# Optimization experiments

Hardware: AMD Instinct MI355X
Metric: run time of the kernel (lower is better)

Reference implementation:

```python
import jax, jax.numpy as jnp
import numpy as np

B, LS, LT = 32, 64, 64
V_SRC, V_TGT = 32000, 32000
E, H = 512, 512


def setup_inputs() -> dict:
    key = jax.random.key(0)
    ks = jax.random.split(key, 16)
    s = 0.05
    inp = {
        "src": jax.random.randint(ks[0], (B, LS), 0, V_SRC),
        "tgt": jax.random.randint(ks[1], (B, LT), 0, V_TGT),
        # encoder params
        "enc_embed": jax.random.normal(ks[2], (V_SRC, E), jnp.float32) * s,
        "enc_wih": jax.random.normal(ks[3], (E, H), jnp.float32) * s,
        "enc_bih": jax.random.normal(ks[4], (H,), jnp.float32) * s,
        "enc_whh": jax.random.normal(ks[5], (H, H), jnp.float32) * s,
        "enc_bhh": jax.random.normal(ks[6], (H,), jnp.float32) * s,
        # decoder params
        "dec_embed": jax.random.normal(ks[7], (V_TGT, E), jnp.float32) * s,
        "dec_wih": jax.random.normal(ks[8], (E, H), jnp.float32) * s,
        "dec_bih": jax.random.normal(ks[9], (H,), jnp.float32) * s,
        "dec_whh": jax.random.normal(ks[10], (H, H), jnp.float32) * s,
        "dec_bhh": jax.random.normal(ks[11], (H,), jnp.float32) * s,
        "h2o_w": jax.random.normal(ks[12], (H, V_TGT), jnp.float32) * s,
        "h2o_b": jax.random.normal(ks[13], (V_TGT,), jnp.float32) * s,
    }
    return inp


def _rnn_scan(tokens, embed, wih, bih, whh, bhh, h0):
    # tokens: (N, L) int; returns (final hidden (N,H), all hiddens (L,N,H))
    xs = embed[tokens].transpose(1, 0, 2)  # (L, N, E)

    def step(h, x):
        h = jnp.tanh(x @ wih + bih + h @ whh + bhh)
        return h, h

    h_last, hs = jax.lax.scan(step, h0, xs)
    return h_last, hs


def reference(src, tgt, enc_embed, enc_wih, enc_bih, enc_whh, enc_bhh,
              dec_embed, dec_wih, dec_bih, dec_whh, dec_bhh, h2o_w, h2o_b):
    n = src.shape[0]
    h0 = jnp.zeros((n, enc_whh.shape[0]), dtype=enc_whh.dtype)
    # encoder: tanh RNN over src, keep only final hidden (teacher-forced training path)
    hidden, _ = _rnn_scan(src, enc_embed, enc_wih, enc_bih, enc_whh, enc_bhh, h0)
    # decoder: tanh RNN over tgt with teacher forcing
    _, dec_hs = _rnn_scan(tgt, dec_embed, dec_wih, dec_bih, dec_whh, dec_bhh, hidden)  # (Lt, N, H)
    # per-step h2o + LogSoftmax, batched over all steps at once (same math)
    logits = dec_hs @ h2o_w + h2o_b  # (Lt, N, V)
    outputs = jax.nn.log_softmax(logits, axis=-1).transpose(1, 0, 2)  # (N, Lt, V)
    return outputs
```

## Files before the change

kernel.cpp:

```cpp
#include <hip/hip_runtime.h>

#define Bd 32
#define Ld 64
#define Hd 512
#define Vd 32000

typedef __bf16 bf16_t;
typedef __bf16 bf16x8 __attribute__((ext_vector_type(8)));
typedef float  f32x4  __attribute__((ext_vector_type(4)));

__global__ void k_pre(
    const int* __restrict__ src, const int* __restrict__ tgt,
    const float* __restrict__ enc_embed, const float* __restrict__ enc_wih,
    const float* __restrict__ enc_bih, const float* __restrict__ enc_bhh,
    const float* __restrict__ dec_embed, const float* __restrict__ dec_wih,
    const float* __restrict__ dec_bih, const float* __restrict__ dec_bhh,
    float* __restrict__ Aenc, float* __restrict__ Adec)
{
    const int tid = threadIdx.x;
    const int bid = blockIdx.x;
    __shared__ float sm[16 * Hd];
    __shared__ int tokl[16];

    const bool isDec = bid >= 128;
    const int rb = (isDec ? bid - 128 : bid) << 4;
    const int*   toks = isDec ? tgt : src;
    const float* emb  = isDec ? dec_embed : enc_embed;
    const float* wih  = isDec ? dec_wih : enc_wih;
    const float* bi   = isDec ? dec_bih : enc_bih;
    const float* bh   = isDec ? dec_bhh : enc_bhh;
    float*       A    = isDec ? Adec : Aenc;
    if (tid < 16) {
        int r = rb + tid;
        tokl[tid] = toks[(r & 31) * Ld + (r >> 5)];
    }
    __syncthreads();
    #pragma unroll
    for (int u = 0; u < 8; ++u) {
        int f = tid + (u << 8);
        int row = f >> 7, c4 = f & 127;
        ((float4*)sm)[f] = ((const float4*)(emb + (size_t)tokl[row] * Hd))[c4];
    }
    __syncthreads();
    const int j0 = tid, j1 = tid + 256;
    float acc0[16], acc1[16];
    #pragma unroll
    for (int r = 0; r < 16; ++r) { acc0[r] = 0.f; acc1[r] = 0.f; }
    #pragma unroll 4
    for (int k = 0; k < Hd; ++k) {
        float w0 = wih[(size_t)k * Hd + j0];
        float w1 = wih[(size_t)k * Hd + j1];
        #pragma unroll
        for (int r = 0; r < 16; ++r) {
            float x = sm[r * Hd + k];
            acc0[r] += x * w0;
            acc1[r] += x * w1;
        }
    }
    float bb0 = bi[j0] + bh[j0], bb1 = bi[j1] + bh[j1];
    #pragma unroll
    for (int r = 0; r < 16; ++r) {
        A[(size_t)(rb + r) * Hd + j0] = acc0[r] + bb0;
        A[(size_t)(rb + r) * Hd + j1] = acc1[r] + bb1;
    }
}

__global__ __launch_bounds__(256, 1) void k_rec(
    const float* __restrict__ enc_whh, const float* __restrict__ dec_whh,
    const float* __restrict__ Aenc, const float* __restrict__ Adec,
    unsigned long long* __restrict__ encX, unsigned long long* __restrict__ decX,
    bf16_t* __restrict__ dhsB)
{
    const int tid = threadIdx.x;
    const int bid = blockIdx.x;
    const int c = bid & 31, p = bid >> 5;
    const int lane = tid & 63, q = tid >> 6;
    const int jb = p << 6;
    const int j = jb + lane;
    __shared__ float hl[Hd];
    __shared__ float part[256];

    {
        float wE[128];
        #pragma unroll
        for (int i = 0; i < 128; ++i) wE[i] = enc_whh[(size_t)(q * 128 + i) * Hd + j];
        for (int t = 0; t < Ld; ++t) {
            float aval = (tid < 64) ? Aenc[(size_t)(t * Bd + c) * Hd + jb + tid] : 0.f;
            if (t == 0) {
                hl[tid] = 0.f; hl[tid + 256] = 0.f;
            } else {
                const unsigned long long* xs = encX + (size_t)(((t - 1) & 1) * Bd + c) * Hd;
                const unsigned want = (unsigned)(t - 1);
                unsigned long long v0 = __hip_atomic_load(xs + tid,       __ATOMIC_RELAXED, __HIP_MEMORY_SCOPE_AGENT);
                unsigned long long v1 = __hip_atomic_load(xs + tid + 256, __ATOMIC_RELAXED, __HIP_MEMORY_SCOPE_AGENT);
                while ((unsigned)(v0 >> 32) != want || (unsigned)(v1 >> 32) != want) {
                    __builtin_amdgcn_s_sleep(1);
                    if ((unsigned)(v0 >> 32) != want)
                        v0 = __hip_atomic_load(xs + tid,       __ATOMIC_RELAXED, __HIP_MEMORY_SCOPE_AGENT);
                    if ((unsigned)(v1 >> 32) != want)
                        v1 = __hip_atomic_load(xs + tid + 256, __ATOMIC_RELAXED, __HIP_MEMORY_SCOPE_AGENT);
                }
                union { unsigned u; float f; } c0, c1;
                c0.u = (unsigned)v0; c1.u = (unsigned)v1;
                hl[tid] = c0.f; hl[tid + 256] = c1.f;
            }
            __syncthreads();
            float acc = 0.f;
            #pragma unroll
            for (int i = 0; i < 128; ++i) acc += wE[i] * hl[q * 128 + i];
            part[tid] = acc;
            __syncthreads();
            if (tid < 64) {
                float s4 = part[tid] + part[tid + 64] + part[tid + 128] + part[tid + 192];
                float h = tanhf(aval + s4);
                union { float f; unsigned u; } cv; cv.f = h;
                unsigned long long pv = ((unsigned long long)(unsigned)t << 32) | cv.u;
                __hip_atomic_store(encX + (size_t)((t & 1) * Bd + c) * Hd + jb + tid, pv,
                                   __ATOMIC_RELAXED, __HIP_MEMORY_SCOPE_AGENT);
            }
            __syncthreads();
        }
    }
    {
        float wD[128];
        #pragma unroll
        for (int i = 0; i < 128; ++i) wD[i] = dec_whh[(size_t)(q * 128 + i) * Hd + j];
        for (int s = 0; s < Ld; ++s) {
            float aval = (tid < 64) ? Adec[(size_t)(s * Bd + c) * Hd + jb + tid] : 0.f;
            {
                const unsigned long long* xs = (s == 0)
                    ? (encX + (size_t)(((Ld - 1) & 1) * Bd + c) * Hd)
                    : (decX + (size_t)(((s - 1) & 1) * Bd + c) * Hd);
                const unsigned want = (s == 0) ? (unsigned)(Ld - 1) : (unsigned)(64 + s - 1);
                unsigned long long v0 = __hip_atomic_load(xs + tid,       __ATOMIC_RELAXED, __HIP_MEMORY_SCOPE_AGENT);
                unsigned long long v1 = __hip_atomic_load(xs + tid + 256, __ATOMIC_RELAXED, __HIP_MEMORY_SCOPE_AGENT);
                while ((unsigned)(v0 >> 32) != want || (unsigned)(v1 >> 32) != want) {
                    __builtin_amdgcn_s_sleep(1);
                    if ((unsigned)(v0 >> 32) != want)
                        v0 = __hip_atomic_load(xs + tid,       __ATOMIC_RELAXED, __HIP_MEMORY_SCOPE_AGENT);
                    if ((unsigned)(v1 >> 32) != want)
                        v1 = __hip_atomic_load(xs + tid + 256, __ATOMIC_RELAXED, __HIP_MEMORY_SCOPE_AGENT);
                }
                union { unsigned u; float f; } c0, c1;
                c0.u = (unsigned)v0; c1.u = (unsigned)v1;
                hl[tid] = c0.f; hl[tid + 256] = c1.f;
            }
            __syncthreads();
            float acc = 0.f;
            #pragma unroll
            for (int i = 0; i < 128; ++i) acc += wD[i] * hl[q * 128 + i];
            part[tid] = acc;
            __syncthreads();
            if (tid < 64) {
                float s4 = part[tid] + part[tid + 64] + part[tid + 128] + part[tid + 192];
                float h = tanhf(aval + s4);
                union { float f; unsigned u; } cv; cv.f = h;
                unsigned long long pv = ((unsigned long long)(unsigned)(64 + s) << 32) | cv.u;
                __hip_atomic_store(decX + (size_t)((s & 1) * Bd + c) * Hd + jb + tid, pv,
                                   __ATOMIC_RELAXED, __HIP_MEMORY_SCOPE_AGENT);
                dhsB[((size_t)c * Ld + s) * Hd + jb + tid] = (bf16_t)h;
            }
            __syncthreads();
        }
    }
}

__global__ void k_wcvt(const float* __restrict__ w, bf16_t* __restrict__ wT)
{
    __shared__ float ls[64][65];
    const int tid = threadIdx.x;
    const int v0 = blockIdx.x << 6;
    const int k0 = blockIdx.y << 6;
    #pragma unroll
    for (int u = 0; u < 16; ++u) {
        int f = tid + (u << 8);
        int r = f >> 6, cc = f & 63;
        ls[r][cc] = w[(size_t)(k0 + r) * Vd + v0 + cc];
    }
    __syncthreads();
    #pragma unroll
    for (int u = 0; u < 16; ++u) {
        int f = tid + (u << 8);
        int vr = f >> 6, kk = f & 63;
        wT[(size_t)(v0 + vr) * Hd + k0 + kk] = (bf16_t)ls[kk][vr];
    }
}

__global__ __launch_bounds__(256, 2) void k_gemm(
    const bf16_t* __restrict__ Amat, const bf16_t* __restrict__ Bmat,
    const float* __restrict__ bias, float* __restrict__ out)
{
    __shared__ bf16_t At[128 * 32];
    __shared__ bf16_t Bt[128 * 32];
    const int tid = threadIdx.x;
    const int n0 = blockIdx.x << 7;
    const int v0 = blockIdx.y << 7;
    const int w = tid >> 6, lane = tid & 63;
    const int l15 = lane & 15, q8 = lane >> 4;
    const int moff = (w & 1) << 6, voff = (w >> 1) << 6;

    f32x4 acc[4][4];
    #pragma unroll
    for (int mi = 0; mi < 4; ++mi)
        #pragma unroll
        for (int vi = 0; vi < 4; ++vi)
            acc[mi][vi] = f32x4{0.f, 0.f, 0.f, 0.f};

    for (int kb = 0; kb < 16; ++kb) {
        __syncthreads();
        #pragma unroll
        for (int u = 0; u < 2; ++u) {
            int f = tid + (u << 8);
            int row = f >> 2, sub = f & 3;
            int subw = sub ^ (row & 3);
            uint4 av = *(const uint4*)(Amat + ((size_t)(n0 + row) * Hd + (kb << 5) + (sub << 3)));
            *(uint4*)(At + row * 32 + (subw << 3)) = av;
            uint4 bv = *(const uint4*)(Bmat + ((size_t)(v0 + row) * Hd + (kb << 5) + (sub << 3)));
            *(uint4*)(Bt + row * 32 + (subw << 3)) = bv;
        }
        __syncthreads();
        bf16x8 af[4], bfr[4];
        #pragma unroll
        for (int mi = 0; mi < 4; ++mi) {
            int m = moff + (mi << 4) + l15;
            af[mi] = *(const bf16x8*)(At + m * 32 + (((q8 ^ (m & 3)) & 3) << 3));
        }
        #pragma unroll
        for (int vi = 0; vi < 4; ++vi) {
            int vv = voff + (vi << 4) + l15;
            bfr[vi] = *(const bf16x8*)(Bt + vv * 32 + (((q8 ^ (vv & 3)) & 3) << 3));
        }
        #pragma unroll
        for (int mi = 0; mi < 4; ++mi)
            #pragma unroll
            for (int vi = 0; vi < 4; ++vi)
                acc[mi][vi] = __builtin_amdgcn_mfma_f32_16x16x32_bf16(af[mi], bfr[vi], acc[mi][vi], 0, 0, 0);
    }
    #pragma unroll
    for (int vi = 0; vi < 4; ++vi) {
        int col = v0 + voff + (vi << 4) + l15;
        float bz = bias[col];
        #pragma unroll
        for (int mi = 0; mi < 4; ++mi) {
            int row = n0 + moff + (mi << 4) + (q8 << 2);
            #pragma unroll
            for (int r = 0; r < 4; ++r)
                out[(size_t)(row + r) * Vd + col] = acc[mi][vi][r] + bz;
        }
    }
}

__global__ void k_logz(const float* __restrict__ out, float* __restrict__ logZ)
{
    const int n = blockIdx.x, tid = threadIdx.x;
    const float* row = out + (size_t)n * Vd;
    float m = -3.4e38f, l = 0.f;
    for (int i = 0; i < 125; ++i) {
        float x = row[i * 256 + tid];
        float nm = fmaxf(m, x);
        l = l * __expf(m - nm) + __expf(x - nm);
        m = nm;
    }
    __shared__ float smx[256], sl[256];
    smx[tid] = m; sl[tid] = l;
    __syncthreads();
    for (int s2 = 128; s2 > 0; s2 >>= 1) {
        if (tid < s2) {
            float m1 = smx[tid], l1 = sl[tid];
            float m2 = smx[tid + s2], l2 = sl[tid + s2];
            float nm = fmaxf(m1, m2);
            sl[tid] = l1 * __expf(m1 - nm) + l2 * __expf(m2 - nm);
            smx[tid] = nm;
        }
        __syncthreads();
    }
    if (tid == 0) logZ[n] = smx[0] + __logf(sl[0]);
}

__global__ void k_sub(float* __restrict__ out, const float* __restrict__ logZ)
{
    int i4 = blockIdx.x * 256 + threadIdx.x;
    int n = i4 / 8000;
    float z = logZ[n];
    float4 x = ((const float4*)out)[i4];
    x.x -= z; x.y -= z; x.z -= z; x.w -= z;
    ((float4*)out)[i4] = x;
}

extern "C" void kernel_launch(void* const* d_in, const int* in_sizes, int n_in,
                              void* d_out, int out_size, void* d_ws, size_t ws_size,
                              hipStream_t stream)
{
    const int*   src       = (const int*)d_in[0];
    const int*   tgt       = (const int*)d_in[1];
    const float* enc_embed = (const float*)d_in[2];
    const float* enc_wih   = (const float*)d_in[3];
    const float* enc_bih   = (const float*)d_in[4];
    const float* enc_whh   = (const float*)d_in[5];
    const float* enc_bhh   = (const float*)d_in[6];
    const float* dec_embed = (const float*)d_in[7];
    const float* dec_wih   = (const float*)d_in[8];
    const float* dec_bih   = (const float*)d_in[9];
    const float* dec_whh   = (const float*)d_in[10];
    const float* dec_bhh   = (const float*)d_in[11];
    const float* h2o_w     = (const float*)d_in[12];
    const float* h2o_b     = (const float*)d_in[13];
    float* out = (float*)d_out;

    char* ws = (char*)d_ws;
    float*  Aenc  = (float*)(ws);
    float*  Adec  = (float*)(ws + ((size_t)4 << 20));
    unsigned long long* encX = (unsigned long long*)(ws + ((size_t)8 << 20));
    unsigned long long* decX = (unsigned long long*)(ws + ((size_t)8 << 20) + (256 << 10));
    bf16_t* dhsB  = (bf16_t*)(ws + ((size_t)9 << 20));
    bf16_t* wT    = (bf16_t*)(ws + ((size_t)12 << 20));
    float*  logZ  = (float*)(ws + ((size_t)44 << 20));

    hipMemsetAsync(ws + ((size_t)8 << 20), 0xFF, (size_t)512 << 10, stream);

    k_wcvt<<<dim3(500, 8), 256, 0, stream>>>(h2o_w, wT);
    k_pre<<<256, 256, 0, stream>>>(src, tgt,
        enc_embed, enc_wih, enc_bih, enc_bhh,
        dec_embed, dec_wih, dec_bih, dec_bhh, Aenc, Adec);
    k_rec<<<256, 256, 0, stream>>>(enc_whh, dec_whh, Aenc, Adec,
        encX, decX, dhsB);
    k_gemm<<<dim3(16, 250), 256, 0, stream>>>(dhsB, wT, h2o_b, out);
    k_logz<<<dim3(2048), 256, 0, stream>>>(out, logZ);
    k_sub<<<64000, 256, 0, stream>>>(out, logZ);
}
```

Measured before the change: 874.1 us.

## Fuse softmax stats into GEMM epilogue, merge prep kernels, restructure recurrence reduction

The memset, the weight transpose/convert and the input projection are merged into one launch. The recurrence kernel now spreads each column's K-reduction over lanes of a wave, combining with shuffles instead of a shared-memory partial buffer, and double-buffers the hidden state so one barrier per step is removed. The GEMM epilogue computes per-tile row max and sum-exp and writes them as partials. This replaces the separate full-row logZ pass, which reread the whole logits array, with one kernel that merges the partials and subtracts. Extra epilogue shuffles and register pressure in the GEMM are the trade-off.

New measurement: 858.4 us. No clear change (-1.8%).

```diff
diff --git a/kernel.cpp b/kernel.cpp
--- a/kernel.cpp
+++ b/kernel.cpp
@@ -9,59 +9,87 @@
 typedef __bf16 bf16x8 __attribute__((ext_vector_type(8)));
 typedef float  f32x4  __attribute__((ext_vector_type(4)));
 
-__global__ void k_pre(
+__global__ void k_prep(
     const int* __restrict__ src, const int* __restrict__ tgt,
     const float* __restrict__ enc_embed, const float* __restrict__ enc_wih,
     const float* __restrict__ enc_bih, const float* __restrict__ enc_bhh,
     const float* __restrict__ dec_embed, const float* __restrict__ dec_wih,
     const float* __restrict__ dec_bih, const float* __restrict__ dec_bhh,
-    float* __restrict__ Aenc, float* __restrict__ Adec)
-{
+    float* __restrict__ Aenc, float* __restrict__ Adec,
+    const float* __restrict__ w, bf16_t* __restrict__ wT,
+    unsigned long long* __restrict__ encX, unsigned long long* __restrict__ decX)
+{
+    __shared__ __align__(16) char smraw[33024];
     const int tid = threadIdx.x;
     const int bid = blockIdx.x;
-    __shared__ float sm[16 * Hd];
-    __shared__ int tokl[16];
-
-    const bool isDec = bid >= 128;
-    const int rb = (isDec ? bid - 128 : bid) << 4;
-    const int*   toks = isDec ? tgt : src;
-    const float* emb  = isDec ? dec_embed : enc_embed;
-    const float* wih  = isDec ? dec_wih : enc_wih;
-    const float* bi   = isDec ? dec_bih : enc_bih;
-    const float* bh   = isDec ? dec_bhh : enc_bhh;
-    float*       A    = isDec ? Adec : Aenc;
-    if (tid < 16) {
-        int r = rb + tid;
-        tokl[tid] = toks[(r & 31) * Ld + (r >> 5)];
-    }
-    __syncthreads();
-    #pragma unroll
-    for (int u = 0; u < 8; ++u) {
-        int f = tid + (u << 8);
-        int row = f >> 7, c4 = f & 127;
-        ((float4*)sm)[f] = ((const float4*)(emb + (size_t)tokl[row] * Hd))[c4];
-    }
-    __syncthreads();
-    const int j0 = tid, j1 = tid + 256;
-    float acc0[16], acc1[16];
-    #pragma unroll
-    for (int r = 0; r < 16; ++r) { acc0[r] = 0.f; acc1[r] = 0.f; }
-    #pragma unroll 4
-    for (int k = 0; k < Hd; ++k) {
-        float w0 = wih[(size_t)k * Hd + j0];
-        float w1 = wih[(size_t)k * Hd + j1];
+
+    if (bid < 256) {
+        {
+            unsigned wgi = ((unsigned)bid << 8) + tid;
+            if (wgi < 32768) encX[wgi] = ~0ull;
+            else             decX[wgi - 32768] = ~0ull;
+        }
+        float* sm  = (float*)smraw;
+        int*  tokl = (int*)(smraw + 32768);
+        const bool isDec = bid >= 128;
+        const int rb = (isDec ? bid - 128 : bid) << 4;
+        const int*   toks = isDec ? tgt : src;
+        const float* emb  = isDec ? dec_embed : enc_embed;
+        const float* wih  = isDec ? dec_wih : enc_wih;
+        const float* bi   = isDec ? dec_bih : enc_bih;
+        const float* bh   = isDec ? dec_bhh : enc_bhh;
+        float*       A    = isDec ? Adec : Aenc;
+        if (tid < 16) {
+            int r = rb + tid;
+            tokl[tid] = toks[(r & 31) * Ld + (r >> 5)];
+        }
+        __syncthreads();
+        #pragma unroll
+        for (int u = 0; u < 8; ++u) {
+            int f = tid + (u << 8);
+            int row = f >> 7, c4 = f & 127;
+            ((float4*)sm)[f] = ((const float4*)(emb + (size_t)tokl[row] * Hd))[c4];
+        }
+        __syncthreads();
+        const int j0 = tid, j1 = tid + 256;
+        float acc0[16], acc1[16];
+        #pragma unroll
+        for (int r = 0; r < 16; ++r) { acc0[r] = 0.f; acc1[r] = 0.f; }
+        #pragma unroll 4
+        for (int k = 0; k < Hd; ++k) {
+            float w0 = wih[(size_t)k * Hd + j0];
+            float w1 = wih[(size_t)k * Hd + j1];
+            #pragma unroll
+            for (int r = 0; r < 16; ++r) {
+                float x = sm[r * Hd + k];
+                acc0[r] += x * w0;
+                acc1[r] += x * w1;
+            }
+        }
+        float bb0 = bi[j0] + bh[j0], bb1 = bi[j1] + bh[j1];
         #pragma unroll
         for (int r = 0; r < 16; ++r) {
-            float x = sm[r * Hd + k];
-            acc0[r] += x * w0;
-            acc1[r] += x * w1;
-        }
-    }
-    float bb0 = bi[j0] + bh[j0], bb1 = bi[j1] + bh[j1];
-    #pragma unroll
-    for (int r = 0; r < 16; ++r) {
-        A[(size_t)(rb + r) * Hd + j0] = acc0[r] + bb0;
-        A[(size_t)(rb + r) * Hd + j1] = acc1[r] + bb1;
+            A[(size_t)(rb + r) * Hd + j0] = acc0[r] + bb0;
+            A[(size_t)(rb + r) * Hd + j1] = acc1[r] + bb1;
+        }
+    } else {
+        float (*ls)[65] = (float(*)[65])smraw;
+        const int b2 = bid - 256;
+        const int v0 = (b2 % 500) << 6;
+        const int k0 = (b2 / 500) << 6;
+        #pragma unroll
+        for (int u = 0; u < 16; ++u) {
+            int f = tid + (u << 8);
+            int r = f >> 6, cc = f & 63;
+            ls[r][cc] = w[(size_t)(k0 + r) * Vd + v0 + cc];
+        }
+        __syncthreads();
+        #pragma unroll
+        for (int u = 0; u < 16; ++u) {
+            int f = tid + (u << 8);
+            int vr = f >> 6, kk = f & 63;
+            wT[(size_t)(v0 + vr) * Hd + k0 + kk] = (bf16_t)ls[kk][vr];
+        }
     }
 }
 
@@ -74,20 +102,22 @@
     const int tid = threadIdx.x;
     const int bid = blockIdx.x;
     const int c = bid & 31, p = bid >> 5;
-    const int lane = tid & 63, q = tid >> 6;
+    const int q = tid >> 6, lane = tid & 63;
+    const int l4 = lane & 15, g = lane >> 4;
     const int jb = p << 6;
-    const int j = jb + lane;
-    __shared__ float hl[Hd];
-    __shared__ float part[256];
+    const int col = jb + (q << 4) + l4;
+    const int i0 = g << 7;
+    __shared__ float hl[2][Hd];
 
     {
         float wE[128];
         #pragma unroll
-        for (int i = 0; i < 128; ++i) wE[i] = enc_whh[(size_t)(q * 128 + i) * Hd + j];
+        for (int i = 0; i < 128; ++i) wE[i] = enc_whh[(size_t)(i0 + i) * Hd + col];
         for (int t = 0; t < Ld; ++t) {
-            float aval = (tid < 64) ? Aenc[(size_t)(t * Bd + c) * Hd + jb + tid] : 0.f;
+            const int par = (t + 1) & 1;
+            float aval = (lane < 16) ? Aenc[(size_t)(t * Bd + c) * Hd + col] : 0.f;
             if (t == 0) {
-                hl[tid] = 0.f; hl[tid + 256] = 0.f;
+                hl[par][tid] = 0.f; hl[par][tid + 256] = 0.f;
             } else {
                 const unsigned long long* xs = encX + (size_t)(((t - 1) & 1) * Bd + c) * Hd;
                 const unsigned want = (unsigned)(t - 1);
@@ -102,31 +132,34 @@
                 }
                 union { unsigned u; float f; } c0, c1;
                 c0.u = (unsigned)v0; c1.u = (unsigned)v1;
-                hl[tid] = c0.f; hl[tid + 256] = c1.f;
+                hl[par][tid] = c0.f; hl[par][tid + 256] = c1.f;
             }
             __syncthreads();
+            const float4* h4 = (const float4*)(&hl[par][i0]);
             float acc = 0.f;
             #pragma unroll
-            for (int i = 0; i < 128; ++i) acc += wE[i] * hl[q * 128 + i];
-            part[tid] = acc;
-            __syncthreads();
-            if (tid < 64) {
-                float s4 = part[tid] + part[tid + 64] + part[tid + 128] + part[tid + 192];
-                float h = tanhf(aval + s4);
+            for (int i = 0; i < 32; ++i) {
+                float4 hv = h4[i];
+                acc += wE[4*i]*hv.x + wE[4*i+1]*hv.y + wE[4*i+2]*hv.z + wE[4*i+3]*hv.w;
+            }
+            acc += __shfl_xor(acc, 16, 64);
+            acc += __shfl_xor(acc, 32, 64);
+            if (lane < 16) {
+                float h = tanhf(aval + acc);
                 union { float f; unsigned u; } cv; cv.f = h;
                 unsigned long long pv = ((unsigned long long)(unsigned)t << 32) | cv.u;
-                __hip_atomic_store(encX + (size_t)((t & 1) * Bd + c) * Hd + jb + tid, pv,
+                __hip_atomic_store(encX + (size_t)((t & 1) * Bd + c) * Hd + col, pv,
                                    __ATOMIC_RELAXED, __HIP_MEMORY_SCOPE_AGENT);
             }
-            __syncthreads();
         }
     }
     {
         float wD[128];
         #pragma unroll
-        for (int i = 0; i < 128; ++i) wD[i] = dec_whh[(size_t)(q * 128 + i) * Hd + j];
+        for (int i = 0; i < 128; ++i) wD[i] = dec_whh[(size_t)(i0 + i) * Hd + col];
         for (int s = 0; s < Ld; ++s) {
-            float aval = (tid < 64) ? Adec[(size_t)(s * Bd + c) * Hd + jb + tid] : 0.f;
+            const int par = (s + 1) & 1;
+            float aval = (lane < 16) ? Adec[(size_t)(s * Bd + c) * Hd + col] : 0.f;
             {
                 const unsigned long long* xs = (s == 0)
                     ? (encX + (size_t)(((Ld - 1) & 1) * Bd + c) * Hd)
@@ -143,55 +176,39 @@
                 }
                 union { unsigned u; float f; } c0, c1;
                 c0.u = (unsigned)v0; c1.u = (unsigned)v1;
-                hl[tid] = c0.f; hl[tid + 256] = c1.f;
+                hl[par][tid] = c0.f; hl[par][tid + 256] = c1.f;
             }
             __syncthreads();
+            const float4* h4 = (const float4*)(&hl[par][i0]);
             float acc = 0.f;
             #pragma unroll
-            for (int i = 0; i < 128; ++i) acc += wD[i] * hl[q * 128 + i];
-            part[tid] = acc;
-            __syncthreads();
-            if (tid < 64) {
-                float s4 = part[tid] + part[tid + 64] + part[tid + 128] + part[tid + 192];
-                float h = tanhf(aval + s4);
+            for (int i = 0; i < 32; ++i) {
+                float4 hv = h4[i];
+                acc += wD[4*i]*hv.x + wD[4*i+1]*hv.y + wD[4*i+2]*hv.z + wD[4*i+3]*hv.w;
+            }
+            acc += __shfl_xor(acc, 16, 64);
+            acc += __shfl_xor(acc, 32, 64);
+            if (lane < 16) {
+                float h = tanhf(aval + acc);
                 union { float f; unsigned u; } cv; cv.f = h;
                 unsigned long long pv = ((unsigned long long)(unsigned)(64 + s) << 32) | cv.u;
-                __hip_atomic_store(decX + (size_t)((s & 1) * Bd + c) * Hd + jb + tid, pv,
+                __hip_atomic_store(decX + (size_t)((s & 1) * Bd + c) * Hd + col, pv,
                                    __ATOMIC_RELAXED, __HIP_MEMORY_SCOPE_AGENT);
-                dhsB[((size_t)c * Ld + s) * Hd + jb + tid] = (bf16_t)h;
-            }
-            __syncthreads();
-        }
-    }
-}
-
-__global__ void k_wcvt(const float* __restrict__ w, bf16_t* __restrict__ wT)
-{
-    __shared__ float ls[64][65];
-    const int tid = threadIdx.x;
-    const int v0 = blockIdx.x << 6;
-    const int k0 = blockIdx.y << 6;
-    #pragma unroll
-    for (int u = 0; u < 16; ++u) {
-        int f = tid + (u << 8);
-        int r = f >> 6, cc = f & 63;
-        ls[r][cc] = w[(size_t)(k0 + r) * Vd + v0 + cc];
-    }
-    __syncthreads();
-    #pragma unroll
-    for (int u = 0; u < 16; ++u) {
-        int f = tid + (u << 8);
-        int vr = f >> 6, kk = f & 63;
-        wT[(size_t)(v0 + vr) * Hd + k0 + kk] = (bf16_t)ls[kk][vr];
+                dhsB[((size_t)c * Ld + s) * Hd + col] = (bf16_t)h;
+            }
+        }
     }
 }
 
 __global__ __launch_bounds__(256, 2) void k_gemm(
     const bf16_t* __restrict__ Amat, const bf16_t* __restrict__ Bmat,
-    const float* __restrict__ bias, float* __restrict__ out)
+    const float* __restrict__ bias, float* __restrict__ out,
+    float2* __restrict__ part2)
 {
     __shared__ bf16_t At[128 * 32];
     __shared__ bf16_t Bt[128 * 32];
+    __shared__ float smM[128][2];
+    __shared__ float smL[128][2];
     const int tid = threadIdx.x;
     const int n0 = blockIdx.x << 7;
     const int v0 = blockIdx.y << 7;
@@ -236,32 +253,78 @@
             for (int vi = 0; vi < 4; ++vi)
                 acc[mi][vi] = __builtin_amdgcn_mfma_f32_16x16x32_bf16(af[mi], bfr[vi], acc[mi][vi], 0, 0, 0);
     }
+
+    float bz[4];
+    #pragma unroll
+    for (int vi = 0; vi < 4; ++vi) bz[vi] = bias[v0 + voff + (vi << 4) + l15];
+
+    float rm[16], rl[16];
+    #pragma unroll
+    for (int k = 0; k < 16; ++k) rm[k] = -3.4e38f;
+    #pragma unroll
+    for (int mi = 0; mi < 4; ++mi)
+        #pragma unroll
+        for (int r = 0; r < 4; ++r)
+            #pragma unroll
+            for (int vi = 0; vi < 4; ++vi)
+                rm[mi * 4 + r] = fmaxf(rm[mi * 4 + r], acc[mi][vi][r] + bz[vi]);
+    #pragma unroll
+    for (int mask = 1; mask < 16; mask <<= 1)
+        #pragma unroll
+        for (int k = 0; k < 16; ++k)
+            rm[k] = fmaxf(rm[k], __shfl_xor(rm[k], mask, 64));
+    #pragma unroll
+    for (int k = 0; k < 16; ++k) rl[k] = 0.f;
     #pragma unroll
     for (int vi = 0; vi < 4; ++vi) {
         int col = v0 + voff + (vi << 4) + l15;
-        float bz = bias[col];
         #pragma unroll
         for (int mi = 0; mi < 4; ++mi) {
             int row = n0 + moff + (mi << 4) + (q8 << 2);
             #pragma unroll
-            for (int r = 0; r < 4; ++r)
-                out[(size_t)(row + r) * Vd + col] = acc[mi][vi][r] + bz;
-        }
-    }
-}
-
-__global__ void k_logz(const float* __restrict__ out, float* __restrict__ logZ)
+            for (int r = 0; r < 4; ++r) {
+                float z = acc[mi][vi][r] + bz[vi];
+                out[(size_t)(row + r) * Vd + col] = z;
+                rl[mi * 4 + r] += __expf(z - rm[mi * 4 + r]);
+            }
+        }
+    }
+    #pragma unroll
+    for (int mask = 1; mask < 16; mask <<= 1)
+        #pragma unroll
+        for (int k = 0; k < 16; ++k)
+            rl[k] += __shfl_xor(rl[k], mask, 64);
+
+    if (l15 == 0) {
+        int half = w >> 1;
+        #pragma unroll
+        for (int mi = 0; mi < 4; ++mi)
+            #pragma unroll
+            for (int r = 0; r < 4; ++r) {
+                int rloc = moff + (mi << 4) + (q8 << 2) + r;
+                smM[rloc][half] = rm[mi * 4 + r];
+                smL[rloc][half] = rl[mi * 4 + r];
+            }
+    }
+    __syncthreads();
+    if (tid < 128) {
+        float m0 = smM[tid][0], m1 = smM[tid][1];
+        float l0 = smL[tid][0], l1 = smL[tid][1];
+        float M = fmaxf(m0, m1);
+        float L = l0 * __expf(m0 - M) + l1 * __expf(m1 - M);
+        part2[(size_t)blockIdx.y * 2048 + n0 + tid] = make_float2(M, L);
+    }
+}
+
+__global__ void k_lsub(float* __restrict__ out, const float2* __restrict__ part2)
 {
     const int n = blockIdx.x, tid = threadIdx.x;
-    const float* row = out + (size_t)n * Vd;
+    __shared__ float smx[256], sl[256];
     float m = -3.4e38f, l = 0.f;
-    for (int i = 0; i < 125; ++i) {
-        float x = row[i * 256 + tid];
-        float nm = fmaxf(m, x);
-        l = l * __expf(m - nm) + __expf(x - nm);
-        m = nm;
-    }
-    __shared__ float smx[256], sl[256];
+    if (tid < 250) {
+        float2 pp = part2[(size_t)tid * 2048 + n];
+        m = pp.x; l = pp.y;
+    }
     smx[tid] = m; sl[tid] = l;
     __syncthreads();
     for (int s2 = 128; s2 > 0; s2 >>= 1) {
@@ -274,17 +337,21 @@
         }
         __syncthreads();
     }
-    if (tid == 0) logZ[n] = smx[0] + __logf(sl[0]);
-}
-
-__global__ void k_sub(float* __restrict__ out, const float* __restrict__ logZ)
-{
-    int i4 = blockIdx.x * 256 + threadIdx.x;
-    int n = i4 / 8000;
-    float z = logZ[n];
-    float4 x = ((const float4*)out)[i4];
-    x.x -= z; x.y -= z; x.z -= z; x.w -= z;
-    ((float4*)out)[i4] = x;
+    const float z = smx[0] + __logf(sl[0]);
+    float4* row = (float4*)(out + (size_t)n * Vd);
+    #pragma unroll 4
+    for (int i = 0; i < 31; ++i) {
+        int idx = i * 256 + tid;
+        float4 x = row[idx];
+        x.x -= z; x.y -= z; x.z -= z; x.w -= z;
+        row[idx] = x;
+    }
+    if (tid < 64) {
+        int idx = 7936 + tid;
+        float4 x = row[idx];
+        x.x -= z; x.y -= z; x.z -= z; x.w -= z;
+        row[idx] = x;
+    }
 }
 
 extern "C" void kernel_launch(void* const* d_in, const int* in_sizes, int n_in,
@@ -314,17 +381,14 @@
     unsigned long long* decX = (unsigned long long*)(ws + ((size_t)8 << 20) + (256 << 10));
     bf16_t* dhsB  = (bf16_t*)(ws + ((size_t)9 << 20));
     bf16_t* wT    = (bf16_t*)(ws + ((size_t)12 << 20));
-    float*  logZ  = (float*)(ws + ((size_t)44 << 20));
-
-    hipMemsetAsync(ws + ((size_t)8 << 20), 0xFF, (size_t)512 << 10, stream);
-
-    k_wcvt<<<dim3(500, 8), 256, 0, stream>>>(h2o_w, wT);
-    k_pre<<<256, 256, 0, stream>>>(src, tgt,
+    float2* part2 = (float2*)(ws);
+
+    k_prep<<<4256, 256, 0, stream>>>(src, tgt,
         enc_embed, enc_wih, enc_bih, enc_bhh,
-        dec_embed, dec_wih, dec_bih, dec_bhh, Aenc, Adec);
+        dec_embed, dec_wih, dec_bih, dec_bhh, Aenc, Adec,
+        h2o_w, wT, encX, decX);
     k_rec<<<256, 256, 0, stream>>>(enc_whh, dec_whh, Aenc, Adec,
         encX, decX, dhsB);
-    k_gemm<<<dim3(16, 250), 256, 0, stream>>>(dhsB, wT, h2o_b, out);
-    k_logz<<<dim3(2048), 256, 0, stream>>>(out, logZ);
-    k_sub<<<64000, 256, 0, stream>>>(out, logZ);
-}
+    k_gemm<<<dim3(16, 250), 256, 0, stream>>>(dhsB, wT, h2o_b, out, part2);
+    k_lsub<<<2048, 256, 0, stream>>>(out, part2);
+}
```
